# Kernel tuning notes

Measured on AMD Instinct MI355X. Metric: run time of the kernel, lower is better.

Reference implementation:

```python
import math
import jax, jax.numpy as jnp
import numpy as np

B, T, D_MODEL, H = 2, 2048, 1024, 16
D_HEAD = D_MODEL // H
EPS = 1e-9


def setup_inputs() -> dict:
    key = jax.random.key(0)
    ks = jax.random.split(key, 5)
    std = 1.0 / math.sqrt(D_MODEL)
    return {
        "x": jax.random.normal(ks[0], (B, T, D_MODEL), dtype=jnp.float32),
        "Wq": jax.random.normal(ks[1], (D_MODEL, D_MODEL), dtype=jnp.float32) * std,
        "Wk": jax.random.normal(ks[2], (D_MODEL, D_MODEL), dtype=jnp.float32) * std,
        "Wv": jax.random.normal(ks[3], (D_MODEL, D_MODEL), dtype=jnp.float32) * std,
        "Wo": jax.random.normal(ks[4], (D_MODEL, D_MODEL), dtype=jnp.float32) * std,
    }


def _attention(x, Wq, Wk, Wv, Wo):
    b, t, d = x.shape
    # projections (nn.Linear without bias: y = x @ W^T)
    q = (x @ Wq.T).reshape(b, t, H, D_HEAD).transpose(0, 2, 1, 3)  # (B,H,T,dh)
    k = (x @ Wk.T).reshape(b, t, H, D_HEAD).transpose(0, 2, 1, 3)
    v = (x @ Wv.T).reshape(b, t, H, D_HEAD).transpose(0, 2, 1, 3)
    scale = 1.0 / math.sqrt(D_HEAD)
    scores = jnp.einsum("bhqd,bhkd->bhqk", q, k) * scale  # (B,H,T,T)
    causal = jnp.tril(jnp.ones((t, t), dtype=bool))
    scores = jnp.where(causal[None, None], scores, -jnp.inf)
    # stable softmax with +eps in denominator (matches online-softmax accumulation)
    m = jnp.max(scores, axis=-1, keepdims=True)
    e = jnp.exp(scores - m)
    l = jnp.sum(e, axis=-1, keepdims=True)
    attn_out = jnp.einsum("bhqk,bhkd->bhqd", e, v) / (l + EPS)
    out = attn_out.transpose(0, 2, 1, 3).reshape(b, t, d)
    return out @ Wo.T


def reference(x, Wq, Wk, Wv, Wo):
    return _attention(x, Wq, Wk, Wv, Wo)
```

## Files before the change

kernel.cpp:

```cpp
#include <hip/hip_runtime.h>


typedef __attribute__((ext_vector_type(8))) short bf16x8;
typedef __attribute__((ext_vector_type(4))) short short4v;
typedef __attribute__((ext_vector_type(4))) float f32x4;

#define T_SEQ 2048
#define D_MODEL 1024
#define NHEAD 16
#define DHEAD 64

__device__ inline short f2bf(float f) {
    unsigned u = __float_as_uint(f);
    u += 0x7fffu + ((u >> 16) & 1u);
    return (short)(u >> 16);
}

__device__ inline unsigned long long pack4bf(float a, float b, float c, float d) {
    return (unsigned long long)(unsigned short)f2bf(a)
         | ((unsigned long long)(unsigned short)f2bf(b) << 16)
         | ((unsigned long long)(unsigned short)f2bf(c) << 32)
         | ((unsigned long long)(unsigned short)f2bf(d) << 48);
}

__device__ inline f32x4 mfma16(bf16x8 a, bf16x8 b, f32x4 c) {
    return __builtin_amdgcn_mfma_f32_16x16x32_bf16(a, b, c, 0, 0, 0);
}

__device__ inline void gld_lds16(const short* g, short* l) {
    __builtin_amdgcn_global_load_lds(
        (const __attribute__((address_space(1))) void*)g,
        (__attribute__((address_space(3))) void*)l, 16, 0, 0);
}

__global__ __launch_bounds__(256) void cast_kernel(const float* __restrict__ s,
                                                   short* __restrict__ d, int n) {
    int i = (blockIdx.x * 256 + threadIdx.x) * 4;
    if (i >= n) return;
    float4 v = *(const float4*)(s + i);
    short4v o = { f2bf(v.x), f2bf(v.y), f2bf(v.z), f2bf(v.w) };
    *(short4v*)(d + i) = o;
}

__global__ __launch_bounds__(256) void cast4_kernel(const float* __restrict__ s0,
                                                    const float* __restrict__ s1,
                                                    const float* __restrict__ s2,
                                                    const float* __restrict__ s3,
                                                    short* __restrict__ d) {
    const float* s = (blockIdx.y == 0) ? s0 : (blockIdx.y == 1) ? s1
                   : (blockIdx.y == 2) ? s2 : s3;
    int i = (blockIdx.x * 256 + threadIdx.x) * 4;
    float4 v = *(const float4*)(s + i);
    short4v o = { f2bf(v.x), f2bf(v.y), f2bf(v.z), f2bf(v.w) };
    *(short4v*)(d + blockIdx.y * 1048576 + i) = o;
}

__global__ __launch_bounds__(256, 3) void gemm_qkv(const short* __restrict__ A,
                                                   const short* __restrict__ B,
                                                   short* __restrict__ C0,
                                                   short* __restrict__ C1,
                                                   short* __restrict__ C2,
                                                   int M, int N, int K) {
    __shared__ short As[4096];
    __shared__ short Bs[4096];

    const int tid = threadIdx.x;
    const int wave = tid >> 6, lane = tid & 63;
    const int g = lane >> 4, ln = lane & 15;
    const int mh = wave & 1, nh = wave >> 1;
    const int m_base = blockIdx.x * 128;
    const int n_base = blockIdx.y * 128;
    const int swz8 = 8 * (g ^ ((ln >> 1) & 3));

    const int srow = tid >> 2;
    const int scol = (((tid & 3) ^ ((tid >> 3) & 3))) * 8;
    const short* Ag = A + (long)(m_base + srow) * K + scol;
    const short* Bg = B + (long)(n_base + srow) * K + scol;
    const long r64 = 64 * (long)K;

    f32x4 acc[4][4];
#pragma unroll
    for (int i = 0; i < 4; i++)
#pragma unroll
        for (int j = 0; j < 4; j++) acc[i][j] = (f32x4){0.f, 0.f, 0.f, 0.f};

    for (int k0 = 0; k0 < K; k0 += 32) {
        gld_lds16(Ag + k0, As + tid * 8);
        gld_lds16(Ag + r64 + k0, As + 2048 + tid * 8);
        gld_lds16(Bg + k0, Bs + tid * 8);
        gld_lds16(Bg + r64 + k0, Bs + 2048 + tid * 8);
        __syncthreads();

        bf16x8 a[4], b[4];
#pragma unroll
        for (int mf = 0; mf < 4; mf++)
            a[mf] = *(const bf16x8*)(As + (mh * 64 + mf * 16 + ln) * 32 + swz8);
#pragma unroll
        for (int nf = 0; nf < 4; nf++)
            b[nf] = *(const bf16x8*)(Bs + (nh * 64 + nf * 16 + ln) * 32 + swz8);
#pragma unroll
        for (int mf = 0; mf < 4; mf++)
#pragma unroll
            for (int nf = 0; nf < 4; nf++)
                acc[mf][nf] = mfma16(a[mf], b[nf], acc[mf][nf]);
        __syncthreads();
    }

    const int mat = n_base >> 10;
    if (mat < 2) {
        short* dst = mat == 0 ? C0 : C1;
#pragma unroll
        for (int mf = 0; mf < 4; mf++)
#pragma unroll
            for (int nf = 0; nf < 4; nf++)
#pragma unroll
                for (int r = 0; r < 4; r++) {
                    int row = m_base + mh * 64 + mf * 16 + g * 4 + r;
                    int cc = (n_base & 1023) + nh * 64 + nf * 16 + ln;
                    int b_ = row >> 11, t = row & 2047;
                    int h = cc >> 6, d = cc & 63;
                    dst[(((long)(b_ * NHEAD + h) * T_SEQ + t) << 6) + d] =
                        f2bf(acc[mf][nf][r]);
                }
    } else {
        short* dst = C2;
#pragma unroll
        for (int mf = 0; mf < 4; mf++)
#pragma unroll
            for (int nf = 0; nf < 4; nf++) {
                short4v pk = { f2bf(acc[mf][nf][0]), f2bf(acc[mf][nf][1]),
                               f2bf(acc[mf][nf][2]), f2bf(acc[mf][nf][3]) };
                int cc = (n_base & 1023) + nh * 64 + nf * 16 + ln;
                int row0 = m_base + mh * 64 + mf * 16 + g * 4;
                int b_ = row0 >> 11, t = row0 & 2047;
                *(short4v*)(&dst[((long)(b_ * 1024 + cc) << 11) + t]) = pk;
            }
    }
}

__global__ __launch_bounds__(256, 3) void gemm_out(const short* __restrict__ A,
                                                   const short* __restrict__ B,
                                                   float* __restrict__ C,
                                                   int M, int N, int K) {
    __shared__ short As[4096];
    __shared__ short Bs[2048];

    const int tid = threadIdx.x;
    const int wave = tid >> 6, lane = tid & 63;
    const int g = lane >> 4, ln = lane & 15;
    const int mh = wave & 1, nh = wave >> 1;
    const int m_base = blockIdx.x * 128;
    const int n_base = blockIdx.y * 64;
    const int swz8 = 8 * (g ^ ((ln >> 1) & 3));

    const int srow = tid >> 2;
    const int scol = (((tid & 3) ^ ((tid >> 3) & 3))) * 8;
    const short* Ag = A + (long)(m_base + srow) * K + scol;
    const short* Bg = B + (long)(n_base + srow) * K + scol;
    const long r64 = 64 * (long)K;

    f32x4 acc[4][2];
#pragma unroll
    for (int i = 0; i < 4; i++)
#pragma unroll
        for (int j = 0; j < 2; j++) acc[i][j] = (f32x4){0.f, 0.f, 0.f, 0.f};

    for (int k0 = 0; k0 < K; k0 += 32) {
        gld_lds16(Ag + k0, As + tid * 8);
        gld_lds16(Ag + r64 + k0, As + 2048 + tid * 8);
        gld_lds16(Bg + k0, Bs + tid * 8);
        __syncthreads();

        bf16x8 a[4], b[2];
#pragma unroll
        for (int mf = 0; mf < 4; mf++)
            a[mf] = *(const bf16x8*)(As + (mh * 64 + mf * 16 + ln) * 32 + swz8);
#pragma unroll
        for (int nf = 0; nf < 2; nf++)
            b[nf] = *(const bf16x8*)(Bs + (nh * 32 + nf * 16 + ln) * 32 + swz8);
#pragma unroll
        for (int mf = 0; mf < 4; mf++)
#pragma unroll
            for (int nf = 0; nf < 2; nf++)
                acc[mf][nf] = mfma16(a[mf], b[nf], acc[mf][nf]);
        __syncthreads();
    }

#pragma unroll
    for (int mf = 0; mf < 4; mf++)
#pragma unroll
        for (int nf = 0; nf < 2; nf++)
#pragma unroll
            for (int r = 0; r < 4; r++) {
                int row = m_base + mh * 64 + mf * 16 + g * 4 + r;
                int col = n_base + nh * 32 + nf * 16 + ln;
                C[(long)row * N + col] = acc[mf][nf][r];
            }
}

__global__ __launch_bounds__(256) void flash_attn(const short* __restrict__ Q,
                                                  const short* __restrict__ Kx,
                                                  const short* __restrict__ Vt,
                                                  short* __restrict__ O) {
    __shared__ short Ks[2][4096];
    __shared__ short Vs[2][4096];
    __shared__ short ldsP[4][16][68];

    const int tid = threadIdx.x;
    const int wv = tid >> 6, lane = tid & 63;
    const int g = lane >> 4, ln = lane & 15;
    const int id = blockIdx.x;
    const int qx = 31 - (id >> 5);
    const int bh = id & 31;
    const int swz8 = 8 * (g ^ ((ln >> 1) & 3));

    const short* Kp = Kx + (long)bh * (T_SEQ * DHEAD);
    const short* Vp = Vt + (long)bh * (DHEAD * T_SEQ);

    const int sr = tid >> 2;
    const int sc8 = (((tid & 3) ^ ((tid >> 3) & 3))) * 8;
    const int offK0 = sr * 64 + sc8;
    const long offV0 = (long)sr * T_SEQ + sc8;
    const int ldst = tid * 8;

    const float sc = 0.125f * 1.44269504089f;
    const int nt = qx + 1;
    const int qrow0 = qx * 64 + wv * 16;

    const short* Qp = Q + ((long)bh * T_SEQ + qrow0) * DHEAD;
    bf16x8 qf0 = *(const bf16x8*)(Qp + ln * 64 + 8 * g);
    bf16x8 qf1 = *(const bf16x8*)(Qp + ln * 64 + 32 + 8 * g);

    f32x4 o[4];
#pragma unroll
    for (int nf = 0; nf < 4; nf++) o[nf] = (f32x4){0.f, 0.f, 0.f, 0.f};
    float li = 0.f;

    gld_lds16(Kp + offK0, &Ks[0][ldst]);
    gld_lds16(Kp + offK0 + 32, &Ks[0][2048 + ldst]);
    gld_lds16(Vp + offV0, &Vs[0][ldst]);
    gld_lds16(Vp + offV0 + 32, &Vs[0][2048 + ldst]);

    int buf = 0;
    for (int i = 0; i < nt; i++) {
        __syncthreads();
        if (i + 1 < nt) {
            const int kO = (i + 1) * 4096 + offK0;
            const long vO = offV0 + (i + 1) * 64;
            gld_lds16(Kp + kO, &Ks[buf ^ 1][ldst]);
            gld_lds16(Kp + kO + 32, &Ks[buf ^ 1][2048 + ldst]);
            gld_lds16(Vp + vO, &Vs[buf ^ 1][ldst]);
            gld_lds16(Vp + vO + 32, &Vs[buf ^ 1][2048 + ldst]);
        }

        f32x4 s[4];
#pragma unroll
        for (int j = 0; j < 4; j++) {
            bf16x8 k0 = *(const bf16x8*)(&Ks[buf][(j * 16 + ln) * 32 + swz8]);
            bf16x8 k1 = *(const bf16x8*)(&Ks[buf][2048 + (j * 16 + ln) * 32 + swz8]);
            s[j] = mfma16(k0, qf0, (f32x4){0.f, 0.f, 0.f, 0.f});
            s[j] = mfma16(k1, qf1, s[j]);
        }

        bf16x8 vf[4][2];
#pragma unroll
        for (int nf = 0; nf < 4; nf++) {
            vf[nf][0] = *(const bf16x8*)(&Vs[buf][(nf * 16 + ln) * 32 + swz8]);
            vf[nf][1] = *(const bf16x8*)(&Vs[buf][2048 + (nf * 16 + ln) * 32 + swz8]);
        }

        if (i == nt - 1) {
            const int ql = 16 * wv + ln;
#pragma unroll
            for (int j = 0; j < 4; j++) {
                int kl = 16 * j + 4 * g;
#pragma unroll
                for (int r = 0; r < 4; r++)
                    if (kl + r > ql) s[j][r] = -INFINITY;
            }
        }

#pragma unroll
        for (int j = 0; j < 4; j++) {
            float e0 = __builtin_amdgcn_exp2f(s[j][0] * sc);
            float e1 = __builtin_amdgcn_exp2f(s[j][1] * sc);
            float e2 = __builtin_amdgcn_exp2f(s[j][2] * sc);
            float e3 = __builtin_amdgcn_exp2f(s[j][3] * sc);
            li += (e0 + e1) + (e2 + e3);
            *(unsigned long long*)(&ldsP[wv][ln][16 * j + 4 * g]) =
                pack4bf(e0, e1, e2, e3);
        }

        asm volatile("s_waitcnt lgkmcnt(0)" ::: "memory");
        bf16x8 pa0 = *(const bf16x8*)(&ldsP[wv][ln][8 * g]);
        bf16x8 pa1 = *(const bf16x8*)(&ldsP[wv][ln][32 + 8 * g]);

#pragma unroll
        for (int nf = 0; nf < 4; nf++) {
            o[nf] = mfma16(pa0, vf[nf][0], o[nf]);
            o[nf] = mfma16(pa1, vf[nf][1], o[nf]);
        }
        buf ^= 1;
    }

    li += __shfl_xor(li, 16);
    li += __shfl_xor(li, 32);

    float lr[4];
#pragma unroll
    for (int r = 0; r < 4; r++)
        lr[r] = 1.f / (__shfl(li, 4 * g + r) + 1e-9f);

    const int b = bh >> 4, h = bh & 15;
#pragma unroll
    for (int nf = 0; nf < 4; nf++) {
#pragma unroll
        for (int r = 0; r < 4; r++) {
            int rr = qrow0 + g * 4 + r;
            O[((long)(b * T_SEQ + rr) << 10) + h * 64 + nf * 16 + ln] =
                f2bf(o[nf][r] * lr[r]);
        }
    }
}

extern "C" void kernel_launch(void* const* d_in, const int* in_sizes, int n_in,
                              void* d_out, int out_size, void* d_ws, size_t ws_size,
                              hipStream_t stream) {
    const float* x  = (const float*)d_in[0];
    const float* Wq = (const float*)d_in[1];
    const float* Wk = (const float*)d_in[2];
    const float* Wv = (const float*)d_in[3];
    const float* Wo = (const float*)d_in[4];

    char* ws = (char*)d_ws;
    short* xb  = (short*)(ws + (0ull  << 20));
    short* wqb = (short*)(ws + (8ull  << 20));
    short* wob = (short*)(ws + (14ull << 20));
    short* Qb  = (short*)(ws + (16ull << 20));
    short* Kb  = (short*)(ws + (24ull << 20));
    short* Vtb = (short*)(ws + (32ull << 20));
    short* Ab  = (short*)(ws + (40ull << 20));

    cast_kernel<<<4096, 256, 0, stream>>>(x, xb, 2 * T_SEQ * D_MODEL);
    cast4_kernel<<<dim3(1024, 4), 256, 0, stream>>>(Wq, Wk, Wv, Wo, wqb);

    gemm_qkv<<<dim3(32, 24), 256, 0, stream>>>(xb, wqb, Qb, Kb, Vtb,
                                               4096, 3072, 1024);

    flash_attn<<<1024, 256, 0, stream>>>(Qb, Kb, Vtb, Ab);

    gemm_out<<<dim3(32, 16), 256, 0, stream>>>(Ab, wob, (float*)d_out,
                                               4096, 1024, 1024);
}
```

Baseline: 170.0 us.

## Merge cast kernels, double GEMM K-tile, and give flash attention two query subtiles per wave

The two fp32-to-bf16 cast kernels become one launch. Both GEMMs now stage 64-wide K tiles in shared memory with an 8-way XOR swizzle, which halves the number of barrier pairs per K sweep. Flash attention processes 128 query rows per block, so each wave holds two 16-row subtiles that share every K/V fragment loaded from LDS. The grid is halved and the causal block order is remapped for load balance. This raises register and LDS use per block, which may lower occupancy.

```diff
diff --git a/kernel.cpp b/kernel.cpp
--- a/kernel.cpp
+++ b/kernel.cpp
@@ -33,26 +33,26 @@
         (__attribute__((address_space(3))) void*)l, 16, 0, 0);
 }
 
-__global__ __launch_bounds__(256) void cast_kernel(const float* __restrict__ s,
-                                                   short* __restrict__ d, int n) {
+__global__ __launch_bounds__(256) void cast_all(const float* __restrict__ x,
+                                                const float* __restrict__ w0,
+                                                const float* __restrict__ w1,
+                                                const float* __restrict__ w2,
+                                                const float* __restrict__ w3,
+                                                short* __restrict__ xdst,
+                                                short* __restrict__ wdst) {
     int i = (blockIdx.x * 256 + threadIdx.x) * 4;
-    if (i >= n) return;
-    float4 v = *(const float4*)(s + i);
+    const float* s;
+    short* d;
+    if (blockIdx.y == 0) {
+        s = x + i; d = xdst + i;
+    } else {
+        int m = i >> 20;
+        s = ((m == 0) ? w0 : (m == 1) ? w1 : (m == 2) ? w2 : w3) + (i & 1048575);
+        d = wdst + i;
+    }
+    float4 v = *(const float4*)s;
     short4v o = { f2bf(v.x), f2bf(v.y), f2bf(v.z), f2bf(v.w) };
-    *(short4v*)(d + i) = o;
-}
-
-__global__ __launch_bounds__(256) void cast4_kernel(const float* __restrict__ s0,
-                                                    const float* __restrict__ s1,
-                                                    const float* __restrict__ s2,
-                                                    const float* __restrict__ s3,
-                                                    short* __restrict__ d) {
-    const float* s = (blockIdx.y == 0) ? s0 : (blockIdx.y == 1) ? s1
-                   : (blockIdx.y == 2) ? s2 : s3;
-    int i = (blockIdx.x * 256 + threadIdx.x) * 4;
-    float4 v = *(const float4*)(s + i);
-    short4v o = { f2bf(v.x), f2bf(v.y), f2bf(v.z), f2bf(v.w) };
-    *(short4v*)(d + blockIdx.y * 1048576 + i) = o;
+    *(short4v*)d = o;
 }
 
 __global__ __launch_bounds__(256, 3) void gemm_qkv(const short* __restrict__ A,
@@ -61,8 +61,8 @@
                                                    short* __restrict__ C1,
                                                    short* __restrict__ C2,
                                                    int M, int N, int K) {
-    __shared__ short As[4096];
-    __shared__ short Bs[4096];
+    __shared__ short As[8192];
+    __shared__ short Bs[8192];
 
     const int tid = threadIdx.x;
     const int wave = tid >> 6, lane = tid & 63;
@@ -70,13 +70,12 @@
     const int mh = wave & 1, nh = wave >> 1;
     const int m_base = blockIdx.x * 128;
     const int n_base = blockIdx.y * 128;
-    const int swz8 = 8 * (g ^ ((ln >> 1) & 3));
-
-    const int srow = tid >> 2;
-    const int scol = (((tid & 3) ^ ((tid >> 3) & 3))) * 8;
+
+    const int srow = tid >> 3;
+    const int scol = ((tid & 7) ^ ((tid >> 3) & 7)) * 8;
     const short* Ag = A + (long)(m_base + srow) * K + scol;
     const short* Bg = B + (long)(n_base + srow) * K + scol;
-    const long r64 = 64 * (long)K;
+    const long shK = 32 * (long)K;
 
     f32x4 acc[4][4];
 #pragma unroll
@@ -84,25 +83,33 @@
 #pragma unroll
         for (int j = 0; j < 4; j++) acc[i][j] = (f32x4){0.f, 0.f, 0.f, 0.f};
 
-    for (int k0 = 0; k0 < K; k0 += 32) {
-        gld_lds16(Ag + k0, As + tid * 8);
-        gld_lds16(Ag + r64 + k0, As + 2048 + tid * 8);
-        gld_lds16(Bg + k0, Bs + tid * 8);
-        gld_lds16(Bg + r64 + k0, Bs + 2048 + tid * 8);
-        __syncthreads();
-
-        bf16x8 a[4], b[4];
-#pragma unroll
-        for (int mf = 0; mf < 4; mf++)
-            a[mf] = *(const bf16x8*)(As + (mh * 64 + mf * 16 + ln) * 32 + swz8);
-#pragma unroll
-        for (int nf = 0; nf < 4; nf++)
-            b[nf] = *(const bf16x8*)(Bs + (nh * 64 + nf * 16 + ln) * 32 + swz8);
-#pragma unroll
-        for (int mf = 0; mf < 4; mf++)
-#pragma unroll
-            for (int nf = 0; nf < 4; nf++)
-                acc[mf][nf] = mfma16(a[mf], b[nf], acc[mf][nf]);
+    for (int k0 = 0; k0 < K; k0 += 64) {
+#pragma unroll
+        for (int sh = 0; sh < 4; sh++) {
+            gld_lds16(Ag + sh * shK + k0, As + sh * 2048 + tid * 8);
+            gld_lds16(Bg + sh * shK + k0, Bs + sh * 2048 + tid * 8);
+        }
+        __syncthreads();
+
+#pragma unroll
+        for (int h = 0; h < 2; h++) {
+            bf16x8 a[4], b[4];
+#pragma unroll
+            for (int mf = 0; mf < 4; mf++) {
+                int row = mh * 64 + mf * 16 + ln;
+                a[mf] = *(const bf16x8*)(As + row * 64 + (((4 * h + g) ^ (ln & 7)) * 8));
+            }
+#pragma unroll
+            for (int nf = 0; nf < 4; nf++) {
+                int row = nh * 64 + nf * 16 + ln;
+                b[nf] = *(const bf16x8*)(Bs + row * 64 + (((4 * h + g) ^ (ln & 7)) * 8));
+            }
+#pragma unroll
+            for (int mf = 0; mf < 4; mf++)
+#pragma unroll
+                for (int nf = 0; nf < 4; nf++)
+                    acc[mf][nf] = mfma16(a[mf], b[nf], acc[mf][nf]);
+        }
         __syncthreads();
     }
 
@@ -142,8 +149,8 @@
                                                    const short* __restrict__ B,
                                                    float* __restrict__ C,
                                                    int M, int N, int K) {
-    __shared__ short As[4096];
-    __shared__ short Bs[2048];
+    __shared__ short As[8192];
+    __shared__ short Bs[4096];
 
     const int tid = threadIdx.x;
     const int wave = tid >> 6, lane = tid & 63;
@@ -151,13 +158,12 @@
     const int mh = wave & 1, nh = wave >> 1;
     const int m_base = blockIdx.x * 128;
     const int n_base = blockIdx.y * 64;
-    const int swz8 = 8 * (g ^ ((ln >> 1) & 3));
-
-    const int srow = tid >> 2;
-    const int scol = (((tid & 3) ^ ((tid >> 3) & 3))) * 8;
+
+    const int srow = tid >> 3;
+    const int scol = ((tid & 7) ^ ((tid >> 3) & 7)) * 8;
     const short* Ag = A + (long)(m_base + srow) * K + scol;
     const short* Bg = B + (long)(n_base + srow) * K + scol;
-    const long r64 = 64 * (long)K;
+    const long shK = 32 * (long)K;
 
     f32x4 acc[4][2];
 #pragma unroll
@@ -165,24 +171,34 @@
 #pragma unroll
         for (int j = 0; j < 2; j++) acc[i][j] = (f32x4){0.f, 0.f, 0.f, 0.f};
 
-    for (int k0 = 0; k0 < K; k0 += 32) {
-        gld_lds16(Ag + k0, As + tid * 8);
-        gld_lds16(Ag + r64 + k0, As + 2048 + tid * 8);
-        gld_lds16(Bg + k0, Bs + tid * 8);
-        __syncthreads();
-
-        bf16x8 a[4], b[2];
-#pragma unroll
-        for (int mf = 0; mf < 4; mf++)
-            a[mf] = *(const bf16x8*)(As + (mh * 64 + mf * 16 + ln) * 32 + swz8);
-#pragma unroll
-        for (int nf = 0; nf < 2; nf++)
-            b[nf] = *(const bf16x8*)(Bs + (nh * 32 + nf * 16 + ln) * 32 + swz8);
-#pragma unroll
-        for (int mf = 0; mf < 4; mf++)
-#pragma unroll
-            for (int nf = 0; nf < 2; nf++)
-                acc[mf][nf] = mfma16(a[mf], b[nf], acc[mf][nf]);
+    for (int k0 = 0; k0 < K; k0 += 64) {
+#pragma unroll
+        for (int sh = 0; sh < 4; sh++)
+            gld_lds16(Ag + sh * shK + k0, As + sh * 2048 + tid * 8);
+#pragma unroll
+        for (int sh = 0; sh < 2; sh++)
+            gld_lds16(Bg + sh * shK + k0, Bs + sh * 2048 + tid * 8);
+        __syncthreads();
+
+#pragma unroll
+        for (int h = 0; h < 2; h++) {
+            bf16x8 a[4], b[2];
+#pragma unroll
+            for (int mf = 0; mf < 4; mf++) {
+                int row = mh * 64 + mf * 16 + ln;
+                a[mf] = *(const bf16x8*)(As + row * 64 + (((4 * h + g) ^ (ln & 7)) * 8));
+            }
+#pragma unroll
+            for (int nf = 0; nf < 2; nf++) {
+                int row = nh * 32 + nf * 16 + ln;
+                b[nf] = *(const bf16x8*)(Bs + row * 64 + (((4 * h + g) ^ (ln & 7)) * 8));
+            }
+#pragma unroll
+            for (int mf = 0; mf < 4; mf++)
+#pragma unroll
+                for (int nf = 0; nf < 2; nf++)
+                    acc[mf][nf] = mfma16(a[mf], b[nf], acc[mf][nf]);
+        }
         __syncthreads();
     }
 
@@ -204,13 +220,14 @@
                                                   short* __restrict__ O) {
     __shared__ short Ks[2][4096];
     __shared__ short Vs[2][4096];
-    __shared__ short ldsP[4][16][68];
+    __shared__ short ldsP[4][32][68];
 
     const int tid = threadIdx.x;
     const int wv = tid >> 6, lane = tid & 63;
     const int g = lane >> 4, ln = lane & 15;
     const int id = blockIdx.x;
-    const int qx = 31 - (id >> 5);
+    const int qxi = id >> 5;
+    const int qx = (qxi < 8) ? 15 - qxi : qxi - 8;
     const int bh = id & 31;
     const int swz8 = 8 * (g ^ ((ln >> 1) & 3));
 
@@ -224,17 +241,22 @@
     const int ldst = tid * 8;
 
     const float sc = 0.125f * 1.44269504089f;
-    const int nt = qx + 1;
-    const int qrow0 = qx * 64 + wv * 16;
+    const int nt = 2 * qx + 2;
+    const int qrow0 = qx * 128 + wv * 32;
 
     const short* Qp = Q + ((long)bh * T_SEQ + qrow0) * DHEAD;
-    bf16x8 qf0 = *(const bf16x8*)(Qp + ln * 64 + 8 * g);
-    bf16x8 qf1 = *(const bf16x8*)(Qp + ln * 64 + 32 + 8 * g);
-
-    f32x4 o[4];
-#pragma unroll
-    for (int nf = 0; nf < 4; nf++) o[nf] = (f32x4){0.f, 0.f, 0.f, 0.f};
-    float li = 0.f;
+    bf16x8 qfA0 = *(const bf16x8*)(Qp + ln * 64 + 8 * g);
+    bf16x8 qfA1 = *(const bf16x8*)(Qp + ln * 64 + 32 + 8 * g);
+    bf16x8 qfB0 = *(const bf16x8*)(Qp + (16 + ln) * 64 + 8 * g);
+    bf16x8 qfB1 = *(const bf16x8*)(Qp + (16 + ln) * 64 + 32 + 8 * g);
+
+    f32x4 oA[4], oB[4];
+#pragma unroll
+    for (int nf = 0; nf < 4; nf++) {
+        oA[nf] = (f32x4){0.f, 0.f, 0.f, 0.f};
+        oB[nf] = (f32x4){0.f, 0.f, 0.f, 0.f};
+    }
+    float liA = 0.f, liB = 0.f;
 
     gld_lds16(Kp + offK0, &Ks[0][ldst]);
     gld_lds16(Kp + offK0 + 32, &Ks[0][2048 + ldst]);
@@ -253,13 +275,15 @@
             gld_lds16(Vp + vO + 32, &Vs[buf ^ 1][2048 + ldst]);
         }
 
-        f32x4 s[4];
+        f32x4 sA[4], sB[4];
 #pragma unroll
         for (int j = 0; j < 4; j++) {
             bf16x8 k0 = *(const bf16x8*)(&Ks[buf][(j * 16 + ln) * 32 + swz8]);
             bf16x8 k1 = *(const bf16x8*)(&Ks[buf][2048 + (j * 16 + ln) * 32 + swz8]);
-            s[j] = mfma16(k0, qf0, (f32x4){0.f, 0.f, 0.f, 0.f});
-            s[j] = mfma16(k1, qf1, s[j]);
+            sA[j] = mfma16(k0, qfA0, (f32x4){0.f, 0.f, 0.f, 0.f});
+            sA[j] = mfma16(k1, qfA1, sA[j]);
+            sB[j] = mfma16(k0, qfB0, (f32x4){0.f, 0.f, 0.f, 0.f});
+            sB[j] = mfma16(k1, qfB1, sB[j]);
         }
 
         bf16x8 vf[4][2];
@@ -269,56 +293,77 @@
             vf[nf][1] = *(const bf16x8*)(&Vs[buf][2048 + (nf * 16 + ln) * 32 + swz8]);
         }
 
-        if (i == nt - 1) {
-            const int ql = 16 * wv + ln;
+        if (i >= 2 * qx) {
+            const int rel = (i - 2 * qx) * 64;
+            const int qA = wv * 32 + ln, qB = qA + 16;
 #pragma unroll
             for (int j = 0; j < 4; j++) {
-                int kl = 16 * j + 4 * g;
-#pragma unroll
-                for (int r = 0; r < 4; r++)
-                    if (kl + r > ql) s[j][r] = -INFINITY;
+                int kl = rel + 16 * j + 4 * g;
+#pragma unroll
+                for (int r = 0; r < 4; r++) {
+                    if (kl + r > qA) sA[j][r] = -INFINITY;
+                    if (kl + r > qB) sB[j][r] = -INFINITY;
+                }
             }
         }
 
 #pragma unroll
         for (int j = 0; j < 4; j++) {
-            float e0 = __builtin_amdgcn_exp2f(s[j][0] * sc);
-            float e1 = __builtin_amdgcn_exp2f(s[j][1] * sc);
-            float e2 = __builtin_amdgcn_exp2f(s[j][2] * sc);
-            float e3 = __builtin_amdgcn_exp2f(s[j][3] * sc);
-            li += (e0 + e1) + (e2 + e3);
+            float a0 = __builtin_amdgcn_exp2f(sA[j][0] * sc);
+            float a1 = __builtin_amdgcn_exp2f(sA[j][1] * sc);
+            float a2 = __builtin_amdgcn_exp2f(sA[j][2] * sc);
+            float a3 = __builtin_amdgcn_exp2f(sA[j][3] * sc);
+            liA += (a0 + a1) + (a2 + a3);
             *(unsigned long long*)(&ldsP[wv][ln][16 * j + 4 * g]) =
-                pack4bf(e0, e1, e2, e3);
+                pack4bf(a0, a1, a2, a3);
+            float b0 = __builtin_amdgcn_exp2f(sB[j][0] * sc);
+            float b1 = __builtin_amdgcn_exp2f(sB[j][1] * sc);
+            float b2 = __builtin_amdgcn_exp2f(sB[j][2] * sc);
+            float b3 = __builtin_amdgcn_exp2f(sB[j][3] * sc);
+            liB += (b0 + b1) + (b2 + b3);
+            *(unsigned long long*)(&ldsP[wv][16 + ln][16 * j + 4 * g]) =
+                pack4bf(b0, b1, b2, b3);
         }
 
         asm volatile("s_waitcnt lgkmcnt(0)" ::: "memory");
-        bf16x8 pa0 = *(const bf16x8*)(&ldsP[wv][ln][8 * g]);
-        bf16x8 pa1 = *(const bf16x8*)(&ldsP[wv][ln][32 + 8 * g]);
+        bf16x8 paA0 = *(const bf16x8*)(&ldsP[wv][ln][8 * g]);
+        bf16x8 paA1 = *(const bf16x8*)(&ldsP[wv][ln][32 + 8 * g]);
+        bf16x8 paB0 = *(const bf16x8*)(&ldsP[wv][16 + ln][8 * g]);
+        bf16x8 paB1 = *(const bf16x8*)(&ldsP[wv][16 + ln][32 + 8 * g]);
 
 #pragma unroll
         for (int nf = 0; nf < 4; nf++) {
-            o[nf] = mfma16(pa0, vf[nf][0], o[nf]);
-            o[nf] = mfma16(pa1, vf[nf][1], o[nf]);
+            oA[nf] = mfma16(paA0, vf[nf][0], oA[nf]);
+            oA[nf] = mfma16(paA1, vf[nf][1], oA[nf]);
+            oB[nf] = mfma16(paB0, vf[nf][0], oB[nf]);
+            oB[nf] = mfma16(paB1, vf[nf][1], oB[nf]);
         }
         buf ^= 1;
     }
 
-    li += __shfl_xor(li, 16);
-    li += __shfl_xor(li, 32);
-
-    float lr[4];
-#pragma unroll
-    for (int r = 0; r < 4; r++)
-        lr[r] = 1.f / (__shfl(li, 4 * g + r) + 1e-9f);
+    liA += __shfl_xor(liA, 16);
+    liA += __shfl_xor(liA, 32);
+    liB += __shfl_xor(liB, 16);
+    liB += __shfl_xor(liB, 32);
+
+    float lrA[4], lrB[4];
+#pragma unroll
+    for (int r = 0; r < 4; r++) {
+        lrA[r] = 1.f / (__shfl(liA, 4 * g + r) + 1e-9f);
+        lrB[r] = 1.f / (__shfl(liB, 4 * g + r) + 1e-9f);
+    }
 
     const int b = bh >> 4, h = bh & 15;
 #pragma unroll
     for (int nf = 0; nf < 4; nf++) {
 #pragma unroll
         for (int r = 0; r < 4; r++) {
-            int rr = qrow0 + g * 4 + r;
-            O[((long)(b * T_SEQ + rr) << 10) + h * 64 + nf * 16 + ln] =
-                f2bf(o[nf][r] * lr[r]);
+            int rrA = qrow0 + 4 * g + r;
+            O[((long)(b * T_SEQ + rrA) << 10) + h * 64 + nf * 16 + ln] =
+                f2bf(oA[nf][r] * lrA[r]);
+            int rrB = rrA + 16;
+            O[((long)(b * T_SEQ + rrB) << 10) + h * 64 + nf * 16 + ln] =
+                f2bf(oB[nf][r] * lrB[r]);
         }
     }
 }
@@ -341,13 +386,12 @@
     short* Vtb = (short*)(ws + (32ull << 20));
     short* Ab  = (short*)(ws + (40ull << 20));
 
-    cast_kernel<<<4096, 256, 0, stream>>>(x, xb, 2 * T_SEQ * D_MODEL);
-    cast4_kernel<<<dim3(1024, 4), 256, 0, stream>>>(Wq, Wk, Wv, Wo, wqb);
+    cast_all<<<dim3(4096, 2), 256, 0, stream>>>(x, Wq, Wk, Wv, Wo, xb, wqb);
 
     gemm_qkv<<<dim3(32, 24), 256, 0, stream>>>(xb, wqb, Qb, Kb, Vtb,
                                                4096, 3072, 1024);
 
-    flash_attn<<<1024, 256, 0, stream>>>(Qb, Kb, Vtb, Ab);
+    flash_attn<<<512, 256, 0, stream>>>(Qb, Kb, Vtb, Ab);
 
     gemm_out<<<dim3(32, 16), 256, 0, stream>>>(Ab, wob, (float*)d_out,
                                                4096, 1024, 1024);
```

Measured after the change: 185.2 us. 1.09x slower.
